# Kernel tuning notes

Hardware: AMD Instinct MI355X
Metric: run time of the kernel (lower is better)

## Reference

```python
import jax, jax.numpy as jnp
import numpy as np

N = 100000
E = 3200000
IN_CH = 512
H1 = 16


def setup_inputs() -> dict:
    key = jax.random.key(0)
    ks = jax.random.split(key, 9)
    x = jax.random.normal(ks[0], (N, IN_CH), dtype=jnp.float32)
    edge_index = jax.random.randint(ks[1], (2, E), 0, N, dtype=jnp.int64)
    # GCNConv params: weight [in, out], bias [out]
    def glorot(k, fan_in, fan_out):
        lim = (6.0 / (fan_in + fan_out)) ** 0.5
        return jax.random.uniform(k, (fan_in, fan_out), jnp.float32, -lim, lim)
    W1 = glorot(ks[2], IN_CH, H1)
    b1 = jnp.zeros((H1,), jnp.float32)
    W2 = glorot(ks[3], H1, H1)
    b2 = jnp.zeros((H1,), jnp.float32)
    W3 = glorot(ks[4], H1, 1)
    b3 = jnp.zeros((1,), jnp.float32)
    return {"x": x, "edge_index": edge_index, "W1": W1, "b1": b1,
            "W2": W2, "b2": b2, "W3": W3, "b3": b3}


def _gcn_conv(x, W, b, src, dst, deg_isqrt):
    # GCNConv: h = X W; out = D^-1/2 (A + I) D^-1/2 h + b
    h = x @ W  # [N, out]
    norm = deg_isqrt[src] * deg_isqrt[dst]  # [E]
    msg = h[src] * norm[:, None]  # gather + scale
    agg = jax.ops.segment_sum(msg, dst, num_segments=N)  # scatter-add
    agg = agg + h * (deg_isqrt * deg_isqrt)[:, None]  # self-loop term
    return agg + b


def reference(x, edge_index, W1, b1, W2, b2, W3, b3):
    src, dst = edge_index[0], edge_index[1]
    # degree of A + I, counted on destination nodes (symmetric norm)
    deg = jax.ops.segment_sum(jnp.ones((E,), jnp.float32), dst, num_segments=N) + 1.0
    deg_isqrt = jax.lax.rsqrt(deg)
    h = _gcn_conv(x, W1, b1, src, dst, deg_isqrt)
    h = jax.nn.relu(h)  # dropout is identity at eval
    h = _gcn_conv(h, W2, b2, src, dst, deg_isqrt)
    h = jax.nn.relu(h)
    out = _gcn_conv(h, W3, b3, src, dst, deg_isqrt)
    return out
```

## Files before the change

### kernel.cpp

```cpp
#include <hip/hip_runtime.h>
#include <hip/hip_bf16.h>

static constexpr int N_NODES = 100000;
static constexpr int N_EDGES = 3200000;
static constexpr int IN_CH = 512;
static constexpr int H = 16;
static constexpr int TB = 256;

static constexpr int BN = 256;
static constexpr int NB = (N_NODES + BN - 1) / BN;
static constexpr int CAP = 8960;
static constexpr int CHUNK = 8192;
static constexpr int GRID_SC = (N_EDGES + CHUNK - 1) / CHUNK;
static constexpr int NBLK64 = (N_NODES + 63) / 64;

__global__ void k_init(int* __restrict__ gcur) {
  int b = blockIdx.x * blockDim.x + threadIdx.x;
  if (b < NB) gcur[b] = b * CAP;
}

__global__ void k_cscatter(const int* __restrict__ ei, int* __restrict__ gcur,
                           int* __restrict__ ebuf) {
  __shared__ int cnt[NB];
  __shared__ int gofs[NB];
  int t = threadIdx.x;
  int c0 = blockIdx.x * CHUNK;
  int c1 = min(c0 + CHUNK, N_EDGES);
  for (int b = t; b < NB; b += TB) cnt[b] = 0;
  __syncthreads();
  for (int j = c0 + t; j < c1; j += TB) atomicAdd(&cnt[ei[N_EDGES + j] >> 8], 1);
  __syncthreads();
  for (int b = t; b < NB; b += TB)
    if (cnt[b] > 0) gofs[b] = atomicAdd(&gcur[b], cnt[b]);
  __syncthreads();
  for (int j = c0 + t; j < c1; j += TB) {
    int s = ei[j];
    int d = ei[N_EDGES + j];
    int slot = atomicAdd(&gofs[d >> 8], 1);
    ebuf[slot] = ((d & 255) << 17) | s;
  }
}

__global__ void k_bscan(const int* __restrict__ gcur, int* __restrict__ bbase) {
  __shared__ int c[512];
  __shared__ int s[TB];
  int t = threadIdx.x;
  c[t] = (t < NB) ? gcur[t] - t * CAP : 0;
  int u = t + 256;
  c[u] = (u < NB) ? gcur[u] - u * CAP : 0;
  __syncthreads();
  s[t] = c[2 * t] + c[2 * t + 1];
  __syncthreads();
  for (int off = 1; off < TB; off <<= 1) {
    int v = (t >= off) ? s[t - off] : 0;
    __syncthreads();
    s[t] += v;
    __syncthreads();
  }
  int e = (t == 0) ? 0 : s[t - 1];
  if (2 * t < NB) bbase[2 * t] = e;
  if (2 * t + 1 < NB) bbase[2 * t + 1] = e + c[2 * t];
}

__global__ void k_bsort(const int* __restrict__ gcur, const int* __restrict__ bbase,
                        const int* __restrict__ ebuf, int* __restrict__ ebuf2,
                        int* __restrict__ nrs, float* __restrict__ disq) {
  __shared__ int cnt[BN];
  __shared__ int pre[BN];
  __shared__ int cur[BN];
  int b = blockIdx.x, t = threadIdx.x;
  cnt[t] = 0;
  __syncthreads();
  int beg = b * CAP, end = gcur[b];
  for (int j = beg + t; j < end; j += TB) atomicAdd(&cnt[ebuf[j] >> 17], 1);
  __syncthreads();
  pre[t] = cnt[t];
  __syncthreads();
  for (int off = 1; off < TB; off <<= 1) {
    int v = (t >= off) ? pre[t - off] : 0;
    __syncthreads();
    pre[t] += v;
    __syncthreads();
  }
  int start = bbase[b] + ((t == 0) ? 0 : pre[t - 1]);
  cur[t] = start;
  int node = b * BN + t;
  if (node <= N_NODES) nrs[node] = start;
  if (node < N_NODES) disq[node] = 1.0f / sqrtf((float)cnt[t] + 1.0f);
  __syncthreads();
  for (int j = beg + t; j < end; j += TB) {
    int p = ebuf[j];
    int slot = atomicAdd(&cur[p >> 17], 1);
    ebuf2[slot] = p & 0x1FFFF;
  }
}

__global__ void k_gemm1(const float* __restrict__ x, const float* __restrict__ W,
                        const float* __restrict__ disq,
                        float* __restrict__ hlo, float* __restrict__ hhi) {
  int r = blockIdx.x * blockDim.x + threadIdx.x;
  if (r >= N_NODES) return;
  const float4* xr = (const float4*)(x + (size_t)r * IN_CH);
  float acc[H];
#pragma unroll
  for (int c = 0; c < H; c++) acc[c] = 0.f;
  for (int k4 = 0; k4 < IN_CH / 4; k4++) {
    float4 xv = xr[k4];
    const float* wr = W + k4 * 4 * H;
    float xs[4] = {xv.x, xv.y, xv.z, xv.w};
#pragma unroll
    for (int j = 0; j < 4; j++) {
#pragma unroll
      for (int c = 0; c < H; c++) acc[c] = fmaf(xs[j], wr[j * H + c], acc[c]);
    }
  }
  float dn = disq[r];
  float4* lo = (float4*)(hlo + (size_t)r * 8);
  float4* hi = (float4*)(hhi + (size_t)r * 8);
  lo[0] = make_float4(acc[0] * dn, acc[1] * dn, acc[2] * dn, acc[3] * dn);
  lo[1] = make_float4(acc[4] * dn, acc[5] * dn, acc[6] * dn, acc[7] * dn);
  hi[0] = make_float4(acc[8] * dn, acc[9] * dn, acc[10] * dn, acc[11] * dn);
  hi[1] = make_float4(acc[12] * dn, acc[13] * dn, acc[14] * dn, acc[15] * dn);
}

__global__ void k_gath8(const int* __restrict__ nrs, const int* __restrict__ ebuf2,
                        const float* __restrict__ disq,
                        const float* __restrict__ hlo, const float* __restrict__ hhi,
                        const float* __restrict__ bias, float* __restrict__ agg) {
  int b = blockIdx.x, half = blockIdx.y, t = threadIdx.x;
  const float* hs = half ? hhi : hlo;
  int grp = t >> 3, lane = t & 7;
#pragma unroll
  for (int k = 0; k < 2; k++) {
    int node = b * 64 + grp * 2 + k;
    if (node >= N_NODES) continue;
    int beg = nrs[node], end = nrs[node + 1];
    float acc = 0.f;
    for (int j = beg; j < end; j++) {
      int src = ebuf2[j];
      acc += hs[(size_t)src * 8 + lane];
    }
    float dn = disq[node];
    float r = fmaf(acc + hs[(size_t)node * 8 + lane], dn, bias[half * 8 + lane]);
    agg[(size_t)node * H + half * 8 + lane] = r;
  }
}

__global__ void k_gemm16(const float* __restrict__ agg, const float* __restrict__ W,
                         const float* __restrict__ disq,
                         float* __restrict__ hlo, float* __restrict__ hhi) {
  int r = blockIdx.x * blockDim.x + threadIdx.x;
  if (r >= N_NODES) return;
  const float4* ap = (const float4*)(agg + (size_t)r * H);
  float v[H];
#pragma unroll
  for (int q = 0; q < 4; q++) {
    float4 t = ap[q];
    v[4 * q + 0] = fmaxf(t.x, 0.f);
    v[4 * q + 1] = fmaxf(t.y, 0.f);
    v[4 * q + 2] = fmaxf(t.z, 0.f);
    v[4 * q + 3] = fmaxf(t.w, 0.f);
  }
  float acc[H];
#pragma unroll
  for (int c = 0; c < H; c++) acc[c] = 0.f;
#pragma unroll
  for (int k = 0; k < H; k++) {
#pragma unroll
    for (int c = 0; c < H; c++) acc[c] = fmaf(v[k], W[k * H + c], acc[c]);
  }
  float dn = disq[r];
  float4* lo = (float4*)(hlo + (size_t)r * 8);
  float4* hi = (float4*)(hhi + (size_t)r * 8);
  lo[0] = make_float4(acc[0] * dn, acc[1] * dn, acc[2] * dn, acc[3] * dn);
  lo[1] = make_float4(acc[4] * dn, acc[5] * dn, acc[6] * dn, acc[7] * dn);
  hi[0] = make_float4(acc[8] * dn, acc[9] * dn, acc[10] * dn, acc[11] * dn);
  hi[1] = make_float4(acc[12] * dn, acc[13] * dn, acc[14] * dn, acc[15] * dn);
}

__global__ void k_gemm_last(const float* __restrict__ agg, const float* __restrict__ W,
                            const float* __restrict__ disq, float* __restrict__ hs3) {
  int r = blockIdx.x * blockDim.x + threadIdx.x;
  if (r >= N_NODES) return;
  const float4* ap = (const float4*)(agg + (size_t)r * H);
  float acc = 0.f;
#pragma unroll
  for (int q = 0; q < 4; q++) {
    float4 t = ap[q];
    acc = fmaf(fmaxf(t.x, 0.f), W[4 * q + 0], acc);
    acc = fmaf(fmaxf(t.y, 0.f), W[4 * q + 1], acc);
    acc = fmaf(fmaxf(t.z, 0.f), W[4 * q + 2], acc);
    acc = fmaf(fmaxf(t.w, 0.f), W[4 * q + 3], acc);
  }
  hs3[r] = acc * disq[r];
}

__global__ void k_gath1(const int* __restrict__ nrs, const int* __restrict__ ebuf2,
                        const float* __restrict__ disq, const float* __restrict__ hs3,
                        const float* __restrict__ bias, float* __restrict__ out) {
  int b = blockIdx.x, t = threadIdx.x;
  int grp = t >> 2, lane = t & 3;
  int node = b * 64 + grp;
  if (node >= N_NODES) return;
  int beg = nrs[node], end = nrs[node + 1];
  float acc = 0.f;
  for (int j = beg + lane; j < end; j += 4) acc += hs3[ebuf2[j]];
  acc += __shfl_xor(acc, 1);
  acc += __shfl_xor(acc, 2);
  if (lane == 0) {
    out[node] = fmaf(acc + hs3[node], disq[node], bias[0]);
  }
}

extern "C" void kernel_launch(void* const* d_in, const int* in_sizes, int n_in,
                              void* d_out, int out_size, void* d_ws, size_t ws_size,
                              hipStream_t stream) {
  const float* x = (const float*)d_in[0];
  const int* ei = (const int*)d_in[1];
  const float* W1 = (const float*)d_in[2];
  const float* b1 = (const float*)d_in[3];
  const float* W2 = (const float*)d_in[4];
  const float* b2 = (const float*)d_in[5];
  const float* W3 = (const float*)d_in[6];
  const float* b3 = (const float*)d_in[7];
  float* out = (float*)d_out;

  int* ebuf = (int*)d_ws;
  int* ebuf2 = ebuf + (size_t)NB * CAP;
  int* gcur = ebuf2 + N_EDGES;
  int* bbase = gcur + NB;
  int* nrs = bbase + NB;
  float* disq = (float*)(nrs + N_NODES + 1);
  float* hlo = disq + N_NODES;
  float* hhi = hlo + (size_t)N_NODES * 8;
  float* agg = (float*)ebuf;
  float* hs3 = hlo;

  int gN = (N_NODES + TB - 1) / TB;

  k_init<<<(NB + TB - 1) / TB, TB, 0, stream>>>(gcur);
  k_cscatter<<<GRID_SC, TB, 0, stream>>>(ei, gcur, ebuf);
  k_bscan<<<1, TB, 0, stream>>>(gcur, bbase);
  k_bsort<<<NB, TB, 0, stream>>>(gcur, bbase, ebuf, ebuf2, nrs, disq);

  k_gemm1<<<gN, TB, 0, stream>>>(x, W1, disq, hlo, hhi);
  k_gath8<<<dim3(NBLK64, 2), TB, 0, stream>>>(nrs, ebuf2, disq, hlo, hhi, b1, agg);
  k_gemm16<<<gN, TB, 0, stream>>>(agg, W2, disq, hlo, hhi);
  k_gath8<<<dim3(NBLK64, 2), TB, 0, stream>>>(nrs, ebuf2, disq, hlo, hhi, b2, agg);
  k_gemm_last<<<gN, TB, 0, stream>>>(agg, W3, disq, hs3);
  k_gath1<<<NBLK64, TB, 0, stream>>>(nrs, ebuf2, disq, hs3, b3, out);
}
```

Before: 672.0 us.

## Fuse gather with next-layer GEMM, pad CSR rows to 4, drop bucket scan

Each node's neighbour list is padded to a multiple of four with a dummy zero-row index, so the gather loops can load indices as int4 and run four loads at a time. Per-node start and end are stored explicitly, and each bucket gets a fixed region, which removes the single-block scan kernel. The aggregation of layers 1 and 2 is fused with the following small 16x16 and 16x1 matmuls through shared memory, removing the separate GEMM kernels and the round trip through an agg buffer. gemm1 now runs with 64-thread blocks. The cost is padding writes, a larger workspace, and lower parallelism in the gather because one block handles both halves of the features.

```diff
diff --git a/kernel.cpp b/kernel.cpp
--- a/kernel.cpp
+++ b/kernel.cpp
@@ -10,6 +10,7 @@
 static constexpr int BN = 256;
 static constexpr int NB = (N_NODES + BN - 1) / BN;
 static constexpr int CAP = 8960;
+static constexpr int CAP2 = CAP + 3 * BN;
 static constexpr int CHUNK = 8192;
 static constexpr int GRID_SC = (N_EDGES + CHUNK - 1) / CHUNK;
 static constexpr int NBLK64 = (N_NODES + 63) / 64;
@@ -41,30 +42,9 @@
   }
 }
 
-__global__ void k_bscan(const int* __restrict__ gcur, int* __restrict__ bbase) {
-  __shared__ int c[512];
-  __shared__ int s[TB];
-  int t = threadIdx.x;
-  c[t] = (t < NB) ? gcur[t] - t * CAP : 0;
-  int u = t + 256;
-  c[u] = (u < NB) ? gcur[u] - u * CAP : 0;
-  __syncthreads();
-  s[t] = c[2 * t] + c[2 * t + 1];
-  __syncthreads();
-  for (int off = 1; off < TB; off <<= 1) {
-    int v = (t >= off) ? s[t - off] : 0;
-    __syncthreads();
-    s[t] += v;
-    __syncthreads();
-  }
-  int e = (t == 0) ? 0 : s[t - 1];
-  if (2 * t < NB) bbase[2 * t] = e;
-  if (2 * t + 1 < NB) bbase[2 * t + 1] = e + c[2 * t];
-}
-
-__global__ void k_bsort(const int* __restrict__ gcur, const int* __restrict__ bbase,
-                        const int* __restrict__ ebuf, int* __restrict__ ebuf2,
-                        int* __restrict__ nrs, float* __restrict__ disq) {
+__global__ void k_bsort(const int* __restrict__ gcur, const int* __restrict__ ebuf,
+                        int* __restrict__ ebuf2, int* __restrict__ nrs,
+                        int* __restrict__ nend, float* __restrict__ disq) {
   __shared__ int cnt[BN];
   __shared__ int pre[BN];
   __shared__ int cur[BN];
@@ -74,7 +54,9 @@
   int beg = b * CAP, end = gcur[b];
   for (int j = beg + t; j < end; j += TB) atomicAdd(&cnt[ebuf[j] >> 17], 1);
   __syncthreads();
-  pre[t] = cnt[t];
+  int myc = cnt[t];
+  int ac = (myc + 3) & ~3;
+  pre[t] = ac;
   __syncthreads();
   for (int off = 1; off < TB; off <<= 1) {
     int v = (t >= off) ? pre[t - off] : 0;
@@ -82,11 +64,15 @@
     pre[t] += v;
     __syncthreads();
   }
-  int start = bbase[b] + ((t == 0) ? 0 : pre[t - 1]);
+  int start = b * CAP2 + ((t == 0) ? 0 : pre[t - 1]);
   cur[t] = start;
   int node = b * BN + t;
-  if (node <= N_NODES) nrs[node] = start;
-  if (node < N_NODES) disq[node] = 1.0f / sqrtf((float)cnt[t] + 1.0f);
+  if (node < N_NODES) {
+    nrs[node] = start;
+    nend[node] = start + ac;
+    disq[node] = 1.0f / sqrtf((float)myc + 1.0f);
+    for (int j = start + myc; j < start + ac; j++) ebuf2[j] = N_NODES;
+  }
   __syncthreads();
   for (int j = beg + t; j < end; j += TB) {
     int p = ebuf[j];
@@ -97,9 +83,24 @@
 
 __global__ void k_gemm1(const float* __restrict__ x, const float* __restrict__ W,
                         const float* __restrict__ disq,
-                        float* __restrict__ hlo, float* __restrict__ hhi) {
+                        float* __restrict__ hloA, float* __restrict__ hhiA,
+                        float* __restrict__ hloB, float* __restrict__ hhiB,
+                        float* __restrict__ hs3) {
   int r = blockIdx.x * blockDim.x + threadIdx.x;
-  if (r >= N_NODES) return;
+  if (r > N_NODES) return;
+  if (r == N_NODES) {
+    float4 z = make_float4(0.f, 0.f, 0.f, 0.f);
+    ((float4*)(hloA + (size_t)r * 8))[0] = z;
+    ((float4*)(hloA + (size_t)r * 8))[1] = z;
+    ((float4*)(hhiA + (size_t)r * 8))[0] = z;
+    ((float4*)(hhiA + (size_t)r * 8))[1] = z;
+    ((float4*)(hloB + (size_t)r * 8))[0] = z;
+    ((float4*)(hloB + (size_t)r * 8))[1] = z;
+    ((float4*)(hhiB + (size_t)r * 8))[0] = z;
+    ((float4*)(hhiB + (size_t)r * 8))[1] = z;
+    hs3[r] = 0.f;
+    return;
+  }
   const float4* xr = (const float4*)(x + (size_t)r * IN_CH);
   float acc[H];
 #pragma unroll
@@ -115,101 +116,138 @@
     }
   }
   float dn = disq[r];
-  float4* lo = (float4*)(hlo + (size_t)r * 8);
-  float4* hi = (float4*)(hhi + (size_t)r * 8);
+  float4* lo = (float4*)(hloA + (size_t)r * 8);
+  float4* hi = (float4*)(hhiA + (size_t)r * 8);
   lo[0] = make_float4(acc[0] * dn, acc[1] * dn, acc[2] * dn, acc[3] * dn);
   lo[1] = make_float4(acc[4] * dn, acc[5] * dn, acc[6] * dn, acc[7] * dn);
   hi[0] = make_float4(acc[8] * dn, acc[9] * dn, acc[10] * dn, acc[11] * dn);
   hi[1] = make_float4(acc[12] * dn, acc[13] * dn, acc[14] * dn, acc[15] * dn);
 }
 
-__global__ void k_gath8(const int* __restrict__ nrs, const int* __restrict__ ebuf2,
-                        const float* __restrict__ disq,
-                        const float* __restrict__ hlo, const float* __restrict__ hhi,
-                        const float* __restrict__ bias, float* __restrict__ agg) {
-  int b = blockIdx.x, half = blockIdx.y, t = threadIdx.x;
-  const float* hs = half ? hhi : hlo;
+__global__ void k_gath_mid(const int* __restrict__ nrs, const int* __restrict__ nend,
+                           const int* __restrict__ ebuf2, const float* __restrict__ disq,
+                           const float* __restrict__ inlo, const float* __restrict__ inhi,
+                           const float* __restrict__ W2, const float* __restrict__ bias,
+                           float* __restrict__ outlo, float* __restrict__ outhi) {
+  __shared__ float agg[64 * 16];
+  __shared__ float w[256];
+  int b = blockIdx.x, t = threadIdx.x;
+  w[t] = W2[t];
   int grp = t >> 3, lane = t & 7;
 #pragma unroll
-  for (int k = 0; k < 2; k++) {
-    int node = b * 64 + grp * 2 + k;
-    if (node >= N_NODES) continue;
-    int beg = nrs[node], end = nrs[node + 1];
-    float acc = 0.f;
-    for (int j = beg; j < end; j++) {
-      int src = ebuf2[j];
-      acc += hs[(size_t)src * 8 + lane];
+  for (int ph = 0; ph < 2; ph++) {
+    const float* hs = ph ? inhi : inlo;
+#pragma unroll
+    for (int k = 0; k < 2; k++) {
+      int node = b * 64 + grp * 2 + k;
+      if (node < N_NODES) {
+        int beg = nrs[node], endp = nend[node];
+        float acc = 0.f;
+        for (int j = beg; j < endp; j += 4) {
+          int4 s = *(const int4*)(ebuf2 + j);
+          float a0 = hs[(size_t)s.x * 8 + lane];
+          float a1 = hs[(size_t)s.y * 8 + lane];
+          float a2 = hs[(size_t)s.z * 8 + lane];
+          float a3 = hs[(size_t)s.w * 8 + lane];
+          acc += (a0 + a1) + (a2 + a3);
+        }
+        float dn = disq[node];
+        agg[(grp * 2 + k) * 16 + ph * 8 + lane] =
+            fmaf(acc + hs[(size_t)node * 8 + lane], dn, bias[ph * 8 + lane]);
+      }
+    }
+  }
+  __syncthreads();
+  int nl = t >> 2, q = t & 3;
+  int node = b * 64 + nl;
+  if (node < N_NODES) {
+    float o0 = 0.f, o1 = 0.f, o2 = 0.f, o3 = 0.f;
+#pragma unroll
+    for (int c4 = 0; c4 < 4; c4++) {
+      float4 av = *(const float4*)(agg + nl * 16 + c4 * 4);
+      float vs[4] = {av.x, av.y, av.z, av.w};
+#pragma unroll
+      for (int i2 = 0; i2 < 4; i2++) {
+        float v = fmaxf(vs[i2], 0.f);
+        const float* wr = w + (c4 * 4 + i2) * 16 + q * 4;
+        o0 = fmaf(v, wr[0], o0);
+        o1 = fmaf(v, wr[1], o1);
+        o2 = fmaf(v, wr[2], o2);
+        o3 = fmaf(v, wr[3], o3);
+      }
     }
     float dn = disq[node];
-    float r = fmaf(acc + hs[(size_t)node * 8 + lane], dn, bias[half * 8 + lane]);
-    agg[(size_t)node * H + half * 8 + lane] = r;
-  }
-}
-
-__global__ void k_gemm16(const float* __restrict__ agg, const float* __restrict__ W,
-                         const float* __restrict__ disq,
-                         float* __restrict__ hlo, float* __restrict__ hhi) {
-  int r = blockIdx.x * blockDim.x + threadIdx.x;
-  if (r >= N_NODES) return;
-  const float4* ap = (const float4*)(agg + (size_t)r * H);
-  float v[H];
-#pragma unroll
-  for (int q = 0; q < 4; q++) {
-    float4 t = ap[q];
-    v[4 * q + 0] = fmaxf(t.x, 0.f);
-    v[4 * q + 1] = fmaxf(t.y, 0.f);
-    v[4 * q + 2] = fmaxf(t.z, 0.f);
-    v[4 * q + 3] = fmaxf(t.w, 0.f);
-  }
-  float acc[H];
-#pragma unroll
-  for (int c = 0; c < H; c++) acc[c] = 0.f;
-#pragma unroll
-  for (int k = 0; k < H; k++) {
-#pragma unroll
-    for (int c = 0; c < H; c++) acc[c] = fmaf(v[k], W[k * H + c], acc[c]);
-  }
-  float dn = disq[r];
-  float4* lo = (float4*)(hlo + (size_t)r * 8);
-  float4* hi = (float4*)(hhi + (size_t)r * 8);
-  lo[0] = make_float4(acc[0] * dn, acc[1] * dn, acc[2] * dn, acc[3] * dn);
-  lo[1] = make_float4(acc[4] * dn, acc[5] * dn, acc[6] * dn, acc[7] * dn);
-  hi[0] = make_float4(acc[8] * dn, acc[9] * dn, acc[10] * dn, acc[11] * dn);
-  hi[1] = make_float4(acc[12] * dn, acc[13] * dn, acc[14] * dn, acc[15] * dn);
-}
-
-__global__ void k_gemm_last(const float* __restrict__ agg, const float* __restrict__ W,
-                            const float* __restrict__ disq, float* __restrict__ hs3) {
-  int r = blockIdx.x * blockDim.x + threadIdx.x;
-  if (r >= N_NODES) return;
-  const float4* ap = (const float4*)(agg + (size_t)r * H);
+    float4 r = make_float4(o0 * dn, o1 * dn, o2 * dn, o3 * dn);
+    if (q < 2) *(float4*)(outlo + (size_t)node * 8 + q * 4) = r;
+    else *(float4*)(outhi + (size_t)node * 8 + (q - 2) * 4) = r;
+  }
+}
+
+__global__ void k_gath_last(const int* __restrict__ nrs, const int* __restrict__ nend,
+                            const int* __restrict__ ebuf2, const float* __restrict__ disq,
+                            const float* __restrict__ inlo, const float* __restrict__ inhi,
+                            const float* __restrict__ W3, const float* __restrict__ bias,
+                            float* __restrict__ hs3) {
+  __shared__ float agg[64 * 16];
+  __shared__ float w3[16];
+  int b = blockIdx.x, t = threadIdx.x;
+  if (t < 16) w3[t] = W3[t];
+  int grp = t >> 3, lane = t & 7;
+#pragma unroll
+  for (int ph = 0; ph < 2; ph++) {
+    const float* hs = ph ? inhi : inlo;
+#pragma unroll
+    for (int k = 0; k < 2; k++) {
+      int node = b * 64 + grp * 2 + k;
+      if (node < N_NODES) {
+        int beg = nrs[node], endp = nend[node];
+        float acc = 0.f;
+        for (int j = beg; j < endp; j += 4) {
+          int4 s = *(const int4*)(ebuf2 + j);
+          float a0 = hs[(size_t)s.x * 8 + lane];
+          float a1 = hs[(size_t)s.y * 8 + lane];
+          float a2 = hs[(size_t)s.z * 8 + lane];
+          float a3 = hs[(size_t)s.w * 8 + lane];
+          acc += (a0 + a1) + (a2 + a3);
+        }
+        float dn = disq[node];
+        agg[(grp * 2 + k) * 16 + ph * 8 + lane] =
+            fmaf(acc + hs[(size_t)node * 8 + lane], dn, bias[ph * 8 + lane]);
+      }
+    }
+  }
+  __syncthreads();
+  int nl = t >> 2, q = t & 3;
+  int node = b * 64 + nl;
+  if (node < N_NODES) {
+    float4 av = *(const float4*)(agg + nl * 16 + q * 4);
+    float o = fmaxf(av.x, 0.f) * w3[q * 4 + 0];
+    o = fmaf(fmaxf(av.y, 0.f), w3[q * 4 + 1], o);
+    o = fmaf(fmaxf(av.z, 0.f), w3[q * 4 + 2], o);
+    o = fmaf(fmaxf(av.w, 0.f), w3[q * 4 + 3], o);
+    o += __shfl_xor(o, 1);
+    o += __shfl_xor(o, 2);
+    if (q == 0) hs3[node] = o * disq[node];
+  }
+}
+
+__global__ void k_gath1(const int* __restrict__ nrs, const int* __restrict__ nend,
+                        const int* __restrict__ ebuf2, const float* __restrict__ disq,
+                        const float* __restrict__ hs3, const float* __restrict__ bias,
+                        float* __restrict__ out) {
+  int b = blockIdx.x, t = threadIdx.x;
+  int nl = t >> 2, lane = t & 3;
+  int node = b * 64 + nl;
+  if (node >= N_NODES) return;
+  int beg = nrs[node], endp = nend[node];
   float acc = 0.f;
-#pragma unroll
-  for (int q = 0; q < 4; q++) {
-    float4 t = ap[q];
-    acc = fmaf(fmaxf(t.x, 0.f), W[4 * q + 0], acc);
-    acc = fmaf(fmaxf(t.y, 0.f), W[4 * q + 1], acc);
-    acc = fmaf(fmaxf(t.z, 0.f), W[4 * q + 2], acc);
-    acc = fmaf(fmaxf(t.w, 0.f), W[4 * q + 3], acc);
-  }
-  hs3[r] = acc * disq[r];
-}
-
-__global__ void k_gath1(const int* __restrict__ nrs, const int* __restrict__ ebuf2,
-                        const float* __restrict__ disq, const float* __restrict__ hs3,
-                        const float* __restrict__ bias, float* __restrict__ out) {
-  int b = blockIdx.x, t = threadIdx.x;
-  int grp = t >> 2, lane = t & 3;
-  int node = b * 64 + grp;
-  if (node >= N_NODES) return;
-  int beg = nrs[node], end = nrs[node + 1];
-  float acc = 0.f;
-  for (int j = beg + lane; j < end; j += 4) acc += hs3[ebuf2[j]];
+  for (int j = beg + 4 * lane; j < endp; j += 16) {
+    int4 s = *(const int4*)(ebuf2 + j);
+    acc += (hs3[s.x] + hs3[s.y]) + (hs3[s.z] + hs3[s.w]);
+  }
   acc += __shfl_xor(acc, 1);
   acc += __shfl_xor(acc, 2);
-  if (lane == 0) {
-    out[node] = fmaf(acc + hs3[node], disq[node], bias[0]);
-  }
+  if (lane == 0) out[node] = fmaf(acc + hs3[node], disq[node], bias[0]);
 }
 
 extern "C" void kernel_launch(void* const* d_in, const int* in_sizes, int n_in,
@@ -227,26 +265,23 @@
 
   int* ebuf = (int*)d_ws;
   int* ebuf2 = ebuf + (size_t)NB * CAP;
-  int* gcur = ebuf2 + N_EDGES;
-  int* bbase = gcur + NB;
-  int* nrs = bbase + NB;
-  float* disq = (float*)(nrs + N_NODES + 1);
-  float* hlo = disq + N_NODES;
-  float* hhi = hlo + (size_t)N_NODES * 8;
-  float* agg = (float*)ebuf;
-  float* hs3 = hlo;
-
-  int gN = (N_NODES + TB - 1) / TB;
-
-  k_init<<<(NB + TB - 1) / TB, TB, 0, stream>>>(gcur);
+  int* gcur = ebuf2 + (size_t)NB * CAP2;
+  int* nrs = gcur + NB;
+  int* nend = nrs + N_NODES;
+  int pad = (4 - ((NB + 2 * N_NODES) & 3)) & 3;
+  float* disq = (float*)(nend + N_NODES + pad);
+  float* hloA = disq + N_NODES;
+  float* hhiA = hloA + (size_t)(N_NODES + 1) * 8;
+  float* hloB = hhiA + (size_t)(N_NODES + 1) * 8;
+  float* hhiB = hloB + (size_t)(N_NODES + 1) * 8;
+  float* hs3 = hhiB + (size_t)(N_NODES + 1) * 8;
+
+  k_init<<<(NB + 63) / 64, 64, 0, stream>>>(gcur);
   k_cscatter<<<GRID_SC, TB, 0, stream>>>(ei, gcur, ebuf);
-  k_bscan<<<1, TB, 0, stream>>>(gcur, bbase);
-  k_bsort<<<NB, TB, 0, stream>>>(gcur, bbase, ebuf, ebuf2, nrs, disq);
-
-  k_gemm1<<<gN, TB, 0, stream>>>(x, W1, disq, hlo, hhi);
-  k_gath8<<<dim3(NBLK64, 2), TB, 0, stream>>>(nrs, ebuf2, disq, hlo, hhi, b1, agg);
-  k_gemm16<<<gN, TB, 0, stream>>>(agg, W2, disq, hlo, hhi);
-  k_gath8<<<dim3(NBLK64, 2), TB, 0, stream>>>(nrs, ebuf2, disq, hlo, hhi, b2, agg);
-  k_gemm_last<<<gN, TB, 0, stream>>>(agg, W3, disq, hs3);
-  k_gath1<<<NBLK64, TB, 0, stream>>>(nrs, ebuf2, disq, hs3, b3, out);
-}
+  k_bsort<<<NB, TB, 0, stream>>>(gcur, ebuf, ebuf2, nrs, nend, disq);
+
+  k_gemm1<<<(N_NODES + 64) / 64, 64, 0, stream>>>(x, W1, disq, hloA, hhiA, hloB, hhiB, hs3);
+  k_gath_mid<<<NBLK64, TB, 0, stream>>>(nrs, nend, ebuf2, disq, hloA, hhiA, W2, b1, hloB, hhiB);
+  k_gath_last<<<NBLK64, TB, 0, stream>>>(nrs, nend, ebuf2, disq, hloB, hhiB, W3, b2, hs3);
+  k_gath1<<<NBLK64, TB, 0, stream>>>(nrs, nend, ebuf2, disq, hs3, b3, out);
+}
```

After: 552.4 us. -17.8%, faster.
